# Performance work log

Measured on AMD Instinct MI355X. Metric: run time of the kernel, lower is better.

The kernel has to match this reference:

```python
import jax, jax.numpy as jnp
import numpy as np

N_AGENTS = 5
RNN = 128
ATT = 64
N_ACT = 10
IN_DIM = 256
SIZE = 65535  # multiple of N_AGENTS -> padding branch never taken
TAU = 0.01


def _gru_cell(x, h, w_ih, w_hh, b_ih, b_hh):
    # PyTorch GRUCell math
    gi = x @ w_ih.T + b_ih
    gh = h @ w_hh.T + b_hh
    i_r, i_z, i_n = jnp.split(gi, 3, axis=-1)
    h_r, h_z, h_n = jnp.split(gh, 3, axis=-1)
    r = jax.nn.sigmoid(i_r + h_r)
    z = jax.nn.sigmoid(i_z + h_z)
    n = jnp.tanh(i_n + r * h_n)
    return (1.0 - z) * n + z * h


def _gru_seq(xs, w_ih, w_hh, b_ih, b_hh):
    # xs: [T, B, D]; zero initial hidden, returns all step outputs [T, B, RNN]
    h0 = jnp.zeros((xs.shape[1], RNN), xs.dtype)
    def step(h, x):
        h2 = _gru_cell(x, h, w_ih, w_hh, b_ih, b_hh)
        return h2, h2
    _, ys = jax.lax.scan(step, h0, xs)
    return ys


def setup_inputs():
    key = jax.random.key(0)
    ks = jax.random.split(key, 26)
    def u(k, shape, fan):
        return jax.random.uniform(k, shape, jnp.float32, -1.0, 1.0) / np.sqrt(fan)
    return {
        'obs': jax.random.normal(ks[0], (SIZE, IN_DIM), jnp.float32),
        'hidden_state': jax.random.normal(ks[1], (SIZE, RNN), jnp.float32),
        'enc_w': u(ks[2], (RNN, IN_DIM), IN_DIM), 'enc_b': u(ks[3], (RNN,), IN_DIM),
        'gru_w_ih': u(ks[4], (3 * RNN, RNN), RNN), 'gru_w_hh': u(ks[5], (3 * RNN, RNN), RNN),
        'gru_b_ih': u(ks[6], (3 * RNN,), RNN), 'gru_b_hh': u(ks[7], (3 * RNN,), RNN),
        'bi_w_ih_f': u(ks[8], (3 * RNN, 2 * RNN), RNN), 'bi_w_hh_f': u(ks[9], (3 * RNN, RNN), RNN),
        'bi_b_ih_f': u(ks[10], (3 * RNN,), RNN), 'bi_b_hh_f': u(ks[11], (3 * RNN,), RNN),
        'bi_w_ih_r': u(ks[12], (3 * RNN, 2 * RNN), RNN), 'bi_w_hh_r': u(ks[13], (3 * RNN, RNN), RNN),
        'bi_b_ih_r': u(ks[14], (3 * RNN,), RNN), 'bi_b_hh_r': u(ks[15], (3 * RNN,), RNN),
        'hard_w': u(ks[16], (2, 2 * RNN), 2 * RNN), 'hard_b': u(ks[17], (2,), 2 * RNN),
        'q_w': u(ks[18], (ATT, RNN), RNN),
        'k_w': u(ks[19], (ATT, RNN), RNN),
        'v_w': u(ks[20], (ATT, RNN), RNN), 'v_b': u(ks[21], (ATT,), RNN),
        'dec_w': u(ks[22], (N_ACT, RNN + ATT), RNN + ATT), 'dec_b': u(ks[23], (N_ACT,), RNN + ATT),
    }


def reference(obs, hidden_state, enc_w, enc_b, gru_w_ih, gru_w_hh, gru_b_ih, gru_b_hh,
              bi_w_ih_f, bi_w_hh_f, bi_b_ih_f, bi_b_hh_f,
              bi_w_ih_r, bi_w_hh_r, bi_b_ih_r, bi_b_hh_r,
              hard_w, hard_b, q_w, k_w, v_w, v_b, dec_w, dec_b):
    size = obs.shape[0]
    bpa = size // N_AGENTS  # batch per agent; SIZE is a multiple of N_AGENTS

    x = jax.nn.relu(obs @ enc_w.T + enc_b)
    h_out = _gru_cell(x, hidden_state, gru_w_ih, gru_w_hh, gru_b_ih, gru_b_hh)

    # --- hard attention: pairwise agent features -> bi-GRU -> gumbel-softmax gate ---
    # (computed exactly as in the original; note the original soft_attention
    #  ignores hard_weights, so this does not influence the returned output)
    h = h_out.reshape(bpa, N_AGENTS, RNN)
    nbr = np.array([[j for j in range(N_AGENTS) if j != i] for i in range(N_AGENTS)])  # [n, n-1]
    h_i = jnp.broadcast_to(h[:, :, None, :], (bpa, N_AGENTS, N_AGENTS - 1, RNN))
    h_j = h[:, nbr, :]                              # [bpa, n, n-1, RNN]
    pair = jnp.concatenate([h_i, h_j], axis=-1)     # [bpa, n, n-1, 2*RNN]
    seq = pair.transpose(2, 0, 1, 3).reshape(N_AGENTS - 1, bpa * N_AGENTS, 2 * RNN)
    fwd = _gru_seq(seq, bi_w_ih_f, bi_w_hh_f, bi_b_ih_f, bi_b_hh_f)
    bwd = _gru_seq(seq[::-1], bi_w_ih_r, bi_w_hh_r, bi_b_ih_r, bi_b_hh_r)[::-1]
    h_hard = jnp.concatenate([fwd, bwd], axis=-1)   # [n-1, B, 2*RNN]
    h_hard = h_hard.transpose(1, 0, 2).reshape(-1, 2 * RNN)
    logits = h_hard @ hard_w.T + hard_b             # [B*(n-1), 2]
    u01 = jax.random.uniform(jax.random.key(42), logits.shape, jnp.float32, 1e-10, 1.0)
    gumbel = -jnp.log(-jnp.log(u01))
    gs = jax.nn.softmax((logits + gumbel) / TAU, axis=-1)
    hard_weights = gs[:, 1].reshape(bpa, N_AGENTS, 1, N_AGENTS - 1).transpose(1, 0, 2, 3)
    _ = hard_weights  # unused downstream, matching the original module

    # --- soft attention: original loops per sample doing a 1x1 matmul+softmax;
    #     vectorized here. softmax over a single element is identically 1. ---
    q = h_out @ q_w.T
    k = h_out @ k_w.T
    v = jax.nn.relu(h_out @ v_w.T + v_b)
    score = jnp.sum(q * k, axis=-1, keepdims=True) / np.sqrt(ATT)  # [B,1]
    soft_w = jax.nn.softmax(score, axis=-1)                         # all ones
    x_att = v * soft_w

    final_input = jnp.concatenate([h_out, x_att], axis=-1)
    output = final_input @ dec_w.T + dec_b
    return output, h_out
```

## Files before the change

### kernel.cpp

```cpp
#include <hip/hip_runtime.h>
#include <stdint.h>

#define SIZE 65535

typedef __bf16 bf16x8 __attribute__((ext_vector_type(8)));
typedef float floatx4 __attribute__((ext_vector_type(4)));

#define WS_ENCW 0
#define WS_WIH  32768
#define WS_WHH  81920
#define WS_VW   131072
#define WS_DECW 139264
#define WS_TOTC 17792

__device__ __forceinline__ unsigned short f2bf(float f) {
    union { float f; unsigned int u; } v; v.f = f;
    unsigned int u = v.u;
    return (unsigned short)((u + 0x7fffu + ((u >> 16) & 1u)) >> 16);
}
__device__ __forceinline__ float bf2f(unsigned short b) {
    union { unsigned int u; float f; } v; v.u = ((unsigned int)b) << 16;
    return v.f;
}
__device__ __forceinline__ float sigmf(float x) {
    x = fminf(fmaxf(x, -30.f), 30.f);
    return 1.f / (1.f + __expf(-x));
}
__device__ __forceinline__ float tanhfast(float x) {
    x = fminf(fmaxf(x, -15.f), 15.f);
    float e = __expf(2.f * x);
    return (e - 1.f) / (e + 1.f);
}

union BF8 { bf16x8 v; unsigned short s[8]; };

__device__ __forceinline__ bf16x8 cvt8g(const float* p) {
    float4 a = *reinterpret_cast<const float4*>(p);
    float4 b = *reinterpret_cast<const float4*>(p + 4);
    BF8 r;
    r.s[0] = f2bf(a.x); r.s[1] = f2bf(a.y); r.s[2] = f2bf(a.z); r.s[3] = f2bf(a.w);
    r.s[4] = f2bf(b.x); r.s[5] = f2bf(b.y); r.s[6] = f2bf(b.z); r.s[7] = f2bf(b.w);
    return r.v;
}
__device__ __forceinline__ bf16x8 ld8(const unsigned short* p) {
    return *reinterpret_cast<const bf16x8*>(p);
}

__global__ __launch_bounds__(256) void cvt_weights(
    const float* __restrict__ enc_w, const float* __restrict__ w_ih,
    const float* __restrict__ w_hh, const float* __restrict__ v_w,
    const float* __restrict__ dec_w, unsigned short* __restrict__ ws) {
    int c = blockIdx.x * 256 + threadIdx.x;
    if (c >= WS_TOTC) return;
    const int lane = c & 63;
    const int l = lane & 15;
    const int q = lane >> 4;
    const float* src; int row, col, stride; bool zero = false;
    if (c < 4096) {
        int lt = c >> 6; int nt = lt >> 3, kt = lt & 7;
        row = nt * 16 + l; col = kt * 32 + q * 8; src = enc_w; stride = 256;
    } else if (c < 10240) {
        int lt = (c - 4096) >> 6; int nt = lt / 12; int r2 = lt % 12;
        int g = r2 >> 2, kt = r2 & 3;
        row = g * 128 + nt * 16 + l; col = kt * 32 + q * 8; src = w_ih; stride = 128;
    } else if (c < 16384) {
        int lt = (c - 10240) >> 6; int nt = lt / 12; int r2 = lt % 12;
        int g = r2 >> 2, kt = r2 & 3;
        row = g * 128 + nt * 16 + l; col = kt * 32 + q * 8; src = w_hh; stride = 128;
    } else if (c < 17408) {
        int lt = (c - 16384) >> 6; int nt = lt >> 2, kt = lt & 3;
        row = nt * 16 + l; col = kt * 32 + q * 8; src = v_w; stride = 128;
    } else {
        int kt = (c - 17408) >> 6;
        row = l; col = kt * 32 + q * 8; src = dec_w; stride = 192;
        zero = (l >= 10);
    }
    float4 a, b;
    if (zero) { a = make_float4(0.f,0.f,0.f,0.f); b = a; }
    else {
        const float* p = src + (size_t)row * stride + col;
        a = *reinterpret_cast<const float4*>(p);
        b = *reinterpret_cast<const float4*>(p + 4);
    }
    unsigned short* d = ws + (size_t)c * 8;
    d[0]=f2bf(a.x); d[1]=f2bf(a.y); d[2]=f2bf(a.z); d[3]=f2bf(a.w);
    d[4]=f2bf(b.x); d[5]=f2bf(b.y); d[6]=f2bf(b.z); d[7]=f2bf(b.w);
}

__global__ __launch_bounds__(256, 2) void attn_critic_kernel(
    const float* __restrict__ obs,
    const float* __restrict__ hid,
    const float* __restrict__ enc_b,
    const float* __restrict__ b_ih,
    const float* __restrict__ b_hh,
    const float* __restrict__ v_b,
    const float* __restrict__ dec_b,
    const unsigned short* __restrict__ wsw,
    float* __restrict__ out)
{
    __shared__ __align__(16) unsigned short sA[4][32][136];
    __shared__ __align__(16) unsigned short sV[4][32][72];
    __shared__ __align__(16) float sO[4][32][10];

    const int tid  = threadIdx.x;
    const int wave = tid >> 6;
    const int lane = tid & 63;
    const int l15  = lane & 15;
    const int quad = lane >> 4;
    const int wrow0 = (blockIdx.x * 4 + wave) * 32;

    int rA0 = wrow0 + l15;      rA0 = (rA0 < SIZE) ? rA0 : (SIZE - 1);
    int rA1 = wrow0 + 16 + l15; rA1 = (rA1 < SIZE) ? rA1 : (SIZE - 1);

    bf16x8 aob[2][8], hf[2][4];
    {
        const float* o0 = obs + (size_t)rA0 * 256;
        const float* o1 = obs + (size_t)rA1 * 256;
#pragma unroll
        for (int kt = 0; kt < 8; ++kt) {
            aob[0][kt] = cvt8g(o0 + kt * 32 + quad * 8);
            aob[1][kt] = cvt8g(o1 + kt * 32 + quad * 8);
        }
        const float* h0 = hid + (size_t)rA0 * 128;
        const float* h1 = hid + (size_t)rA1 * 128;
#pragma unroll
        for (int kt = 0; kt < 4; ++kt) {
            hf[0][kt] = cvt8g(h0 + kt * 32 + quad * 8);
            hf[1][kt] = cvt8g(h1 + kt * 32 + quad * 8);
        }
    }
    __builtin_amdgcn_sched_barrier(0);

    {
        const unsigned short* encf = wsw + WS_ENCW + lane * 8;
#pragma unroll 2
        for (int nt = 0; nt < 8; ++nt) {
            floatx4 a0 = floatx4{0.f,0.f,0.f,0.f}, a1 = a0;
#pragma unroll
            for (int kt = 0; kt < 8; ++kt) {
                bf16x8 b = ld8(encf + (size_t)(nt * 8 + kt) * 512);
                a0 = __builtin_amdgcn_mfma_f32_16x16x32_bf16(aob[0][kt], b, a0, 0, 0, 0);
                a1 = __builtin_amdgcn_mfma_f32_16x16x32_bf16(aob[1][kt], b, a1, 0, 0, 0);
            }
            float bias = enc_b[nt * 16 + l15];
#pragma unroll
            for (int r = 0; r < 4; ++r) {
                sA[wave][quad * 4 + r][nt * 16 + l15]      = f2bf(fmaxf(a0[r] + bias, 0.f));
                sA[wave][16 + quad * 4 + r][nt * 16 + l15] = f2bf(fmaxf(a1[r] + bias, 0.f));
            }
        }
    }
    bf16x8 xf[2][4];
#pragma unroll
    for (int kt = 0; kt < 4; ++kt) {
        xf[0][kt] = ld8(&sA[wave][l15][kt * 32 + quad * 8]);
        xf[1][kt] = ld8(&sA[wave][16 + l15][kt * 32 + quad * 8]);
    }

    {
        const unsigned short* wihf = wsw + WS_WIH + lane * 8;
        const unsigned short* whhf = wsw + WS_WHH + lane * 8;
#pragma unroll 1
        for (int nt = 0; nt < 8; ++nt) {
            const int nr = nt * 16 + l15;
            floatx4 gi[3][2], gh[3][2];
#pragma unroll
            for (int g = 0; g < 3; ++g) {
                gi[g][0] = floatx4{0.f,0.f,0.f,0.f}; gi[g][1] = gi[g][0];
                gh[g][0] = gi[g][0]; gh[g][1] = gi[g][0];
            }
#pragma unroll
            for (int g = 0; g < 3; ++g)
#pragma unroll
                for (int kt = 0; kt < 4; ++kt) {
                    bf16x8 bi = ld8(wihf + (size_t)((nt * 3 + g) * 4 + kt) * 512);
                    bf16x8 bh = ld8(whhf + (size_t)((nt * 3 + g) * 4 + kt) * 512);
                    gi[g][0] = __builtin_amdgcn_mfma_f32_16x16x32_bf16(xf[0][kt], bi, gi[g][0], 0, 0, 0);
                    gi[g][1] = __builtin_amdgcn_mfma_f32_16x16x32_bf16(xf[1][kt], bi, gi[g][1], 0, 0, 0);
                    gh[g][0] = __builtin_amdgcn_mfma_f32_16x16x32_bf16(hf[0][kt], bh, gh[g][0], 0, 0, 0);
                    gh[g][1] = __builtin_amdgcn_mfma_f32_16x16x32_bf16(hf[1][kt], bh, gh[g][1], 0, 0, 0);
                }
            const float bir_ = b_ih[nr], biz_ = b_ih[nr + 128], bin_ = b_ih[nr + 256];
            const float bhr_ = b_hh[nr], bhz_ = b_hh[nr + 128], bhn_ = b_hh[nr + 256];
#pragma unroll
            for (int m = 0; m < 2; ++m)
#pragma unroll
                for (int r = 0; r < 4; ++r) {
                    const int grow = wrow0 + m * 16 + quad * 4 + r;
                    const int rowc = (grow < SIZE) ? grow : (SIZE - 1);
                    float hprev = hid[(size_t)rowc * 128 + nr];
                    float rg = sigmf(gi[0][m][r] + bir_ + gh[0][m][r] + bhr_);
                    float zg = sigmf(gi[1][m][r] + biz_ + gh[1][m][r] + bhz_);
                    float ng = tanhfast(gi[2][m][r] + bin_ + rg * (gh[2][m][r] + bhn_));
                    float ho = (1.f - zg) * ng + zg * hprev;
                    sA[wave][m * 16 + quad * 4 + r][nr] = f2bf(ho);
                }
        }
    }

    {
        float* out_h = out + (size_t)SIZE * 10;
#pragma unroll 1
        for (int it = 0; it < 16; ++it) {
            int idx = it * 256 + lane * 4;
            int rr = idx >> 7, cc = idx & 127;
            int grow = wrow0 + rr;
            if (grow < SIZE) {
                float2 p0 = make_float2(bf2f(sA[wave][rr][cc]),     bf2f(sA[wave][rr][cc + 1]));
                float2 p1 = make_float2(bf2f(sA[wave][rr][cc + 2]), bf2f(sA[wave][rr][cc + 3]));
                float* dst = out_h + (size_t)grow * 128 + cc;
                *reinterpret_cast<float2*>(dst)     = p0;
                *reinterpret_cast<float2*>(dst + 2) = p1;
            }
        }
    }

    bf16x8 af[2][4];
#pragma unroll
    for (int kt = 0; kt < 4; ++kt) {
        af[0][kt] = ld8(&sA[wave][l15][kt * 32 + quad * 8]);
        af[1][kt] = ld8(&sA[wave][16 + l15][kt * 32 + quad * 8]);
    }
    {
        const unsigned short* vwf = wsw + WS_VW + lane * 8;
#pragma unroll 1
        for (int nt = 0; nt < 4; ++nt) {
            floatx4 a0 = floatx4{0.f,0.f,0.f,0.f}, a1 = a0;
#pragma unroll
            for (int kt = 0; kt < 4; ++kt) {
                bf16x8 b = ld8(vwf + (size_t)(nt * 4 + kt) * 512);
                a0 = __builtin_amdgcn_mfma_f32_16x16x32_bf16(af[0][kt], b, a0, 0, 0, 0);
                a1 = __builtin_amdgcn_mfma_f32_16x16x32_bf16(af[1][kt], b, a1, 0, 0, 0);
            }
            float bias = v_b[nt * 16 + l15];
#pragma unroll
            for (int r = 0; r < 4; ++r) {
                sV[wave][quad * 4 + r][nt * 16 + l15]      = f2bf(fmaxf(a0[r] + bias, 0.f));
                sV[wave][16 + quad * 4 + r][nt * 16 + l15] = f2bf(fmaxf(a1[r] + bias, 0.f));
            }
        }
    }

    {
        const unsigned short* decf = wsw + WS_DECW + lane * 8;
        floatx4 d0 = floatx4{0.f,0.f,0.f,0.f}, d1 = d0;
#pragma unroll
        for (int kt = 0; kt < 6; ++kt) {
            bf16x8 b = ld8(decf + (size_t)kt * 512);
            bf16x8 a0 = (kt < 4) ? af[0][kt] : ld8(&sV[wave][l15][(kt - 4) * 32 + quad * 8]);
            bf16x8 a1 = (kt < 4) ? af[1][kt] : ld8(&sV[wave][16 + l15][(kt - 4) * 32 + quad * 8]);
            d0 = __builtin_amdgcn_mfma_f32_16x16x32_bf16(a0, b, d0, 0, 0, 0);
            d1 = __builtin_amdgcn_mfma_f32_16x16x32_bf16(a1, b, d1, 0, 0, 0);
        }
        if (l15 < 10) {
            float bias = dec_b[l15];
#pragma unroll
            for (int r = 0; r < 4; ++r) {
                sO[wave][quad * 4 + r][l15]      = d0[r] + bias;
                sO[wave][16 + quad * 4 + r][l15] = d1[r] + bias;
            }
        }
#pragma unroll
        for (int j = 0; j < 5; ++j) {
            int idx = j * 64 + lane;
            int row = idx / 10, col = idx % 10;
            int grow = wrow0 + row;
            if (grow < SIZE)
                out[(size_t)grow * 10 + col] = sO[wave][row][col];
        }
    }
}

extern "C" void kernel_launch(void* const* d_in, const int* in_sizes, int n_in,
                              void* d_out, int out_size, void* d_ws, size_t ws_size,
                              hipStream_t stream) {
    const float* obs   = (const float*)d_in[0];
    const float* hid   = (const float*)d_in[1];
    const float* enc_w = (const float*)d_in[2];
    const float* enc_b = (const float*)d_in[3];
    const float* w_ih  = (const float*)d_in[4];
    const float* w_hh  = (const float*)d_in[5];
    const float* b_ih  = (const float*)d_in[6];
    const float* b_hh  = (const float*)d_in[7];
    const float* v_w   = (const float*)d_in[20];
    const float* v_b   = (const float*)d_in[21];
    const float* dec_w = (const float*)d_in[22];
    const float* dec_b = (const float*)d_in[23];
    unsigned short* wsw = (unsigned short*)d_ws;
    float* out = (float*)d_out;

    hipLaunchKernelGGL(cvt_weights, dim3((WS_TOTC + 255) / 256), dim3(256), 0, stream,
                       enc_w, w_ih, w_hh, v_w, dec_w, wsw);
    hipLaunchKernelGGL(attn_critic_kernel, dim3(512), dim3(256), 0, stream,
                       obs, hid, enc_b, b_ih, b_hh, v_b, dec_b, wsw, out);
}
```

Baseline: 224.1 us.

## Halve rows per wave to 16 and double grid for higher occupancy

Each wave now processes 16 rows instead of 32, halving per-wave register arrays and shared memory. Launch bounds go from 2 to 4 blocks per SM and the grid doubles to 1024 blocks, so more waves can hide memory latency. The cost is that each weight fragment loaded from the workspace now feeds only one MFMA instead of two, which doubles weight traffic per output row.

```diff
diff --git a/kernel.cpp b/kernel.cpp
--- a/kernel.cpp
+++ b/kernel.cpp
@@ -87,7 +87,7 @@
     d[4]=f2bf(b.x); d[5]=f2bf(b.y); d[6]=f2bf(b.z); d[7]=f2bf(b.w);
 }
 
-__global__ __launch_bounds__(256, 2) void attn_critic_kernel(
+__global__ __launch_bounds__(256, 4) void attn_critic_kernel(
     const float* __restrict__ obs,
     const float* __restrict__ hid,
     const float* __restrict__ enc_b,
@@ -98,36 +98,29 @@
     const unsigned short* __restrict__ wsw,
     float* __restrict__ out)
 {
-    __shared__ __align__(16) unsigned short sA[4][32][136];
-    __shared__ __align__(16) unsigned short sV[4][32][72];
-    __shared__ __align__(16) float sO[4][32][10];
+    __shared__ __align__(16) unsigned short sA[4][16][136];
+    __shared__ __align__(16) unsigned short sV[4][16][72];
+    __shared__ __align__(16) float sO[4][16][10];
 
     const int tid  = threadIdx.x;
     const int wave = tid >> 6;
     const int lane = tid & 63;
     const int l15  = lane & 15;
     const int quad = lane >> 4;
-    const int wrow0 = (blockIdx.x * 4 + wave) * 32;
-
-    int rA0 = wrow0 + l15;      rA0 = (rA0 < SIZE) ? rA0 : (SIZE - 1);
-    int rA1 = wrow0 + 16 + l15; rA1 = (rA1 < SIZE) ? rA1 : (SIZE - 1);
-
-    bf16x8 aob[2][8], hf[2][4];
+    const int wrow0 = (blockIdx.x * 4 + wave) * 16;
+
+    int rA0 = wrow0 + l15; rA0 = (rA0 < SIZE) ? rA0 : (SIZE - 1);
+
+    bf16x8 aob[8], hf[4];
     {
         const float* o0 = obs + (size_t)rA0 * 256;
-        const float* o1 = obs + (size_t)rA1 * 256;
-#pragma unroll
-        for (int kt = 0; kt < 8; ++kt) {
-            aob[0][kt] = cvt8g(o0 + kt * 32 + quad * 8);
-            aob[1][kt] = cvt8g(o1 + kt * 32 + quad * 8);
-        }
+#pragma unroll
+        for (int kt = 0; kt < 8; ++kt)
+            aob[kt] = cvt8g(o0 + kt * 32 + quad * 8);
         const float* h0 = hid + (size_t)rA0 * 128;
-        const float* h1 = hid + (size_t)rA1 * 128;
-#pragma unroll
-        for (int kt = 0; kt < 4; ++kt) {
-            hf[0][kt] = cvt8g(h0 + kt * 32 + quad * 8);
-            hf[1][kt] = cvt8g(h1 + kt * 32 + quad * 8);
-        }
+#pragma unroll
+        for (int kt = 0; kt < 4; ++kt)
+            hf[kt] = cvt8g(h0 + kt * 32 + quad * 8);
     }
     __builtin_amdgcn_sched_barrier(0);
 
@@ -135,27 +128,22 @@
         const unsigned short* encf = wsw + WS_ENCW + lane * 8;
 #pragma unroll 2
         for (int nt = 0; nt < 8; ++nt) {
-            floatx4 a0 = floatx4{0.f,0.f,0.f,0.f}, a1 = a0;
+            floatx4 a0 = floatx4{0.f,0.f,0.f,0.f};
 #pragma unroll
             for (int kt = 0; kt < 8; ++kt) {
                 bf16x8 b = ld8(encf + (size_t)(nt * 8 + kt) * 512);
-                a0 = __builtin_amdgcn_mfma_f32_16x16x32_bf16(aob[0][kt], b, a0, 0, 0, 0);
-                a1 = __builtin_amdgcn_mfma_f32_16x16x32_bf16(aob[1][kt], b, a1, 0, 0, 0);
+                a0 = __builtin_amdgcn_mfma_f32_16x16x32_bf16(aob[kt], b, a0, 0, 0, 0);
             }
             float bias = enc_b[nt * 16 + l15];
 #pragma unroll
-            for (int r = 0; r < 4; ++r) {
-                sA[wave][quad * 4 + r][nt * 16 + l15]      = f2bf(fmaxf(a0[r] + bias, 0.f));
-                sA[wave][16 + quad * 4 + r][nt * 16 + l15] = f2bf(fmaxf(a1[r] + bias, 0.f));
-            }
-        }
-    }
-    bf16x8 xf[2][4];
-#pragma unroll
-    for (int kt = 0; kt < 4; ++kt) {
-        xf[0][kt] = ld8(&sA[wave][l15][kt * 32 + quad * 8]);
-        xf[1][kt] = ld8(&sA[wave][16 + l15][kt * 32 + quad * 8]);
-    }
+            for (int r = 0; r < 4; ++r)
+                sA[wave][quad * 4 + r][nt * 16 + l15] = f2bf(fmaxf(a0[r] + bias, 0.f));
+        }
+    }
+    bf16x8 xf[4];
+#pragma unroll
+    for (int kt = 0; kt < 4; ++kt)
+        xf[kt] = ld8(&sA[wave][l15][kt * 32 + quad * 8]);
 
     {
         const unsigned short* wihf = wsw + WS_WIH + lane * 8;
@@ -163,11 +151,11 @@
 #pragma unroll 1
         for (int nt = 0; nt < 8; ++nt) {
             const int nr = nt * 16 + l15;
-            floatx4 gi[3][2], gh[3][2];
+            floatx4 gi[3], gh[3];
 #pragma unroll
             for (int g = 0; g < 3; ++g) {
-                gi[g][0] = floatx4{0.f,0.f,0.f,0.f}; gi[g][1] = gi[g][0];
-                gh[g][0] = gi[g][0]; gh[g][1] = gi[g][0];
+                gi[g] = floatx4{0.f,0.f,0.f,0.f};
+                gh[g] = gi[g];
             }
 #pragma unroll
             for (int g = 0; g < 3; ++g)
@@ -175,33 +163,29 @@
                 for (int kt = 0; kt < 4; ++kt) {
                     bf16x8 bi = ld8(wihf + (size_t)((nt * 3 + g) * 4 + kt) * 512);
                     bf16x8 bh = ld8(whhf + (size_t)((nt * 3 + g) * 4 + kt) * 512);
-                    gi[g][0] = __builtin_amdgcn_mfma_f32_16x16x32_bf16(xf[0][kt], bi, gi[g][0], 0, 0, 0);
-                    gi[g][1] = __builtin_amdgcn_mfma_f32_16x16x32_bf16(xf[1][kt], bi, gi[g][1], 0, 0, 0);
-                    gh[g][0] = __builtin_amdgcn_mfma_f32_16x16x32_bf16(hf[0][kt], bh, gh[g][0], 0, 0, 0);
-                    gh[g][1] = __builtin_amdgcn_mfma_f32_16x16x32_bf16(hf[1][kt], bh, gh[g][1], 0, 0, 0);
+                    gi[g] = __builtin_amdgcn_mfma_f32_16x16x32_bf16(xf[kt], bi, gi[g], 0, 0, 0);
+                    gh[g] = __builtin_amdgcn_mfma_f32_16x16x32_bf16(hf[kt], bh, gh[g], 0, 0, 0);
                 }
             const float bir_ = b_ih[nr], biz_ = b_ih[nr + 128], bin_ = b_ih[nr + 256];
             const float bhr_ = b_hh[nr], bhz_ = b_hh[nr + 128], bhn_ = b_hh[nr + 256];
 #pragma unroll
-            for (int m = 0; m < 2; ++m)
-#pragma unroll
-                for (int r = 0; r < 4; ++r) {
-                    const int grow = wrow0 + m * 16 + quad * 4 + r;
-                    const int rowc = (grow < SIZE) ? grow : (SIZE - 1);
-                    float hprev = hid[(size_t)rowc * 128 + nr];
-                    float rg = sigmf(gi[0][m][r] + bir_ + gh[0][m][r] + bhr_);
-                    float zg = sigmf(gi[1][m][r] + biz_ + gh[1][m][r] + bhz_);
-                    float ng = tanhfast(gi[2][m][r] + bin_ + rg * (gh[2][m][r] + bhn_));
-                    float ho = (1.f - zg) * ng + zg * hprev;
-                    sA[wave][m * 16 + quad * 4 + r][nr] = f2bf(ho);
-                }
+            for (int r = 0; r < 4; ++r) {
+                const int grow = wrow0 + quad * 4 + r;
+                const int rowc = (grow < SIZE) ? grow : (SIZE - 1);
+                float hprev = hid[(size_t)rowc * 128 + nr];
+                float rg = sigmf(gi[0][r] + bir_ + gh[0][r] + bhr_);
+                float zg = sigmf(gi[1][r] + biz_ + gh[1][r] + bhz_);
+                float ng = tanhfast(gi[2][r] + bin_ + rg * (gh[2][r] + bhn_));
+                float ho = (1.f - zg) * ng + zg * hprev;
+                sA[wave][quad * 4 + r][nr] = f2bf(ho);
+            }
         }
     }
 
     {
         float* out_h = out + (size_t)SIZE * 10;
 #pragma unroll 1
-        for (int it = 0; it < 16; ++it) {
+        for (int it = 0; it < 8; ++it) {
             int idx = it * 256 + lane * 4;
             int rr = idx >> 7, cc = idx & 127;
             int grow = wrow0 + rr;
@@ -215,58 +199,51 @@
         }
     }
 
-    bf16x8 af[2][4];
-#pragma unroll
-    for (int kt = 0; kt < 4; ++kt) {
-        af[0][kt] = ld8(&sA[wave][l15][kt * 32 + quad * 8]);
-        af[1][kt] = ld8(&sA[wave][16 + l15][kt * 32 + quad * 8]);
-    }
+    bf16x8 af[4];
+#pragma unroll
+    for (int kt = 0; kt < 4; ++kt)
+        af[kt] = ld8(&sA[wave][l15][kt * 32 + quad * 8]);
     {
         const unsigned short* vwf = wsw + WS_VW + lane * 8;
 #pragma unroll 1
         for (int nt = 0; nt < 4; ++nt) {
-            floatx4 a0 = floatx4{0.f,0.f,0.f,0.f}, a1 = a0;
+            floatx4 a0 = floatx4{0.f,0.f,0.f,0.f};
 #pragma unroll
             for (int kt = 0; kt < 4; ++kt) {
                 bf16x8 b = ld8(vwf + (size_t)(nt * 4 + kt) * 512);
-                a0 = __builtin_amdgcn_mfma_f32_16x16x32_bf16(af[0][kt], b, a0, 0, 0, 0);
-                a1 = __builtin_amdgcn_mfma_f32_16x16x32_bf16(af[1][kt], b, a1, 0, 0, 0);
+                a0 = __builtin_amdgcn_mfma_f32_16x16x32_bf16(af[kt], b, a0, 0, 0, 0);
             }
             float bias = v_b[nt * 16 + l15];
 #pragma unroll
-            for (int r = 0; r < 4; ++r) {
-                sV[wave][quad * 4 + r][nt * 16 + l15]      = f2bf(fmaxf(a0[r] + bias, 0.f));
-                sV[wave][16 + quad * 4 + r][nt * 16 + l15] = f2bf(fmaxf(a1[r] + bias, 0.f));
-            }
+            for (int r = 0; r < 4; ++r)
+                sV[wave][quad * 4 + r][nt * 16 + l15] = f2bf(fmaxf(a0[r] + bias, 0.f));
         }
     }
 
     {
         const unsigned short* decf = wsw + WS_DECW + lane * 8;
-        floatx4 d0 = floatx4{0.f,0.f,0.f,0.f}, d1 = d0;
+        floatx4 d0 = floatx4{0.f,0.f,0.f,0.f};
 #pragma unroll
         for (int kt = 0; kt < 6; ++kt) {
             bf16x8 b = ld8(decf + (size_t)kt * 512);
-            bf16x8 a0 = (kt < 4) ? af[0][kt] : ld8(&sV[wave][l15][(kt - 4) * 32 + quad * 8]);
-            bf16x8 a1 = (kt < 4) ? af[1][kt] : ld8(&sV[wave][16 + l15][(kt - 4) * 32 + quad * 8]);
+            bf16x8 a0 = (kt < 4) ? af[kt] : ld8(&sV[wave][l15][(kt - 4) * 32 + quad * 8]);
             d0 = __builtin_amdgcn_mfma_f32_16x16x32_bf16(a0, b, d0, 0, 0, 0);
-            d1 = __builtin_amdgcn_mfma_f32_16x16x32_bf16(a1, b, d1, 0, 0, 0);
         }
         if (l15 < 10) {
             float bias = dec_b[l15];
 #pragma unroll
-            for (int r = 0; r < 4; ++r) {
-                sO[wave][quad * 4 + r][l15]      = d0[r] + bias;
-                sO[wave][16 + quad * 4 + r][l15] = d1[r] + bias;
-            }
-        }
-#pragma unroll
-        for (int j = 0; j < 5; ++j) {
+            for (int r = 0; r < 4; ++r)
+                sO[wave][quad * 4 + r][l15] = d0[r] + bias;
+        }
+#pragma unroll
+        for (int j = 0; j < 3; ++j) {
             int idx = j * 64 + lane;
-            int row = idx / 10, col = idx % 10;
-            int grow = wrow0 + row;
-            if (grow < SIZE)
-                out[(size_t)grow * 10 + col] = sO[wave][row][col];
+            if (idx < 160) {
+                int row = idx / 10, col = idx % 10;
+                int grow = wrow0 + row;
+                if (grow < SIZE)
+                    out[(size_t)grow * 10 + col] = sO[wave][row][col];
+            }
         }
     }
 }
@@ -291,6 +268,6 @@
 
     hipLaunchKernelGGL(cvt_weights, dim3((WS_TOTC + 255) / 256), dim3(256), 0, stream,
                        enc_w, w_ih, w_hh, v_w, dec_w, wsw);
-    hipLaunchKernelGGL(attn_critic_kernel, dim3(512), dim3(256), 0, stream,
+    hipLaunchKernelGGL(attn_critic_kernel, dim3(1024), dim3(256), 0, stream,
                        obs, hid, enc_b, b_ih, b_hh, v_b, dec_b, wsw, out);
 }
```

After: 223.6 us. No clear change (-0.2%).

## Stage weight fragments into LDS via async global_load_lds double buffering

Applied to the files above, without the earlier changes.

Weight fragments for the encoder, GRU, value and decoder matmuls are now copied cooperatively by all four waves into a double-buffered LDS region using global_load_lds. Each tile is prefetched one step ahead while the current tile feeds the MFMAs. This replaces per-wave redundant global loads of the same weights with a shared copy. The h_out store is also moved after the decoder, and hprev loads are hoisted before the GRU MFMAs. The cost is a block-wide __syncthreads after every weight tile (about 40 barriers) and 16KB more LDS, which may lower occupancy.

```diff
diff --git a/kernel.cpp b/kernel.cpp
--- a/kernel.cpp
+++ b/kernel.cpp
@@ -44,6 +44,24 @@
 }
 __device__ __forceinline__ bf16x8 ld8(const unsigned short* p) {
     return *reinterpret_cast<const bf16x8*>(p);
+}
+
+__device__ __forceinline__ void glds16(const unsigned short* g, unsigned short* l) {
+    __builtin_amdgcn_global_load_lds(
+        (const __attribute__((address_space(1))) unsigned int*)g,
+        (__attribute__((address_space(3))) unsigned int*)l, 16, 0, 0);
+}
+
+__device__ __forceinline__ void stage_seq(unsigned short* dst, const unsigned short* src,
+                                          int nfrags, int wave, int lane) {
+    for (int s = wave; s < nfrags; s += 4)
+        glds16(src + s * 512 + lane * 8, dst + s * 512);
+}
+__device__ __forceinline__ void stage_gru(unsigned short* dst, const unsigned short* wsw,
+                                          int ng, int wave, int lane) {
+    const int fo = (ng * 4 + wave) * 512 + lane * 8;
+    glds16(wsw + WS_WIH + fo, dst + wave * 512);
+    glds16(wsw + WS_WHH + fo, dst + (4 + wave) * 512);
 }
 
 __global__ __launch_bounds__(256) void cvt_weights(
@@ -98,6 +116,7 @@
     const unsigned short* __restrict__ wsw,
     float* __restrict__ out)
 {
+    __shared__ __align__(16) unsigned short wbuf[2][4096];
     __shared__ __align__(16) unsigned short sA[4][32][136];
     __shared__ __align__(16) unsigned short sV[4][32][72];
     __shared__ __align__(16) float sO[4][32][10];
@@ -112,6 +131,8 @@
     int rA0 = wrow0 + l15;      rA0 = (rA0 < SIZE) ? rA0 : (SIZE - 1);
     int rA1 = wrow0 + 16 + l15; rA1 = (rA1 < SIZE) ? rA1 : (SIZE - 1);
 
+    stage_seq(wbuf[0], wsw + WS_ENCW, 8, wave, lane);
+
     bf16x8 aob[2][8], hf[2][4];
     {
         const float* o0 = obs + (size_t)rA0 * 256;
@@ -130,26 +151,29 @@
         }
     }
     __builtin_amdgcn_sched_barrier(0);
-
-    {
-        const unsigned short* encf = wsw + WS_ENCW + lane * 8;
-#pragma unroll 2
-        for (int nt = 0; nt < 8; ++nt) {
-            floatx4 a0 = floatx4{0.f,0.f,0.f,0.f}, a1 = a0;
-#pragma unroll
-            for (int kt = 0; kt < 8; ++kt) {
-                bf16x8 b = ld8(encf + (size_t)(nt * 8 + kt) * 512);
-                a0 = __builtin_amdgcn_mfma_f32_16x16x32_bf16(aob[0][kt], b, a0, 0, 0, 0);
-                a1 = __builtin_amdgcn_mfma_f32_16x16x32_bf16(aob[1][kt], b, a1, 0, 0, 0);
-            }
-            float bias = enc_b[nt * 16 + l15];
-#pragma unroll
-            for (int r = 0; r < 4; ++r) {
-                sA[wave][quad * 4 + r][nt * 16 + l15]      = f2bf(fmaxf(a0[r] + bias, 0.f));
-                sA[wave][16 + quad * 4 + r][nt * 16 + l15] = f2bf(fmaxf(a1[r] + bias, 0.f));
-            }
-        }
-    }
+    __syncthreads();
+
+#pragma unroll 1
+    for (int nt = 0; nt < 8; ++nt) {
+        const int cur = nt & 1;
+        if (nt < 7) stage_seq(wbuf[cur ^ 1], wsw + WS_ENCW + (nt + 1) * 4096, 8, wave, lane);
+        else        stage_gru(wbuf[cur ^ 1], wsw, 0, wave, lane);
+        const float bias = enc_b[nt * 16 + l15];
+        floatx4 a0 = floatx4{0.f,0.f,0.f,0.f}, a1 = a0;
+#pragma unroll
+        for (int kt = 0; kt < 8; ++kt) {
+            bf16x8 b = ld8(&wbuf[cur][kt * 512 + lane * 8]);
+            a0 = __builtin_amdgcn_mfma_f32_16x16x32_bf16(aob[0][kt], b, a0, 0, 0, 0);
+            a1 = __builtin_amdgcn_mfma_f32_16x16x32_bf16(aob[1][kt], b, a1, 0, 0, 0);
+        }
+#pragma unroll
+        for (int r = 0; r < 4; ++r) {
+            sA[wave][quad * 4 + r][nt * 16 + l15]      = f2bf(fmaxf(a0[r] + bias, 0.f));
+            sA[wave][16 + quad * 4 + r][nt * 16 + l15] = f2bf(fmaxf(a1[r] + bias, 0.f));
+        }
+        __syncthreads();
+    }
+
     bf16x8 xf[2][4];
 #pragma unroll
     for (int kt = 0; kt < 4; ++kt) {
@@ -157,44 +181,107 @@
         xf[1][kt] = ld8(&sA[wave][16 + l15][kt * 32 + quad * 8]);
     }
 
+#pragma unroll 1
+    for (int nt = 0; nt < 8; ++nt) {
+        const int nr = nt * 16 + l15;
+        float hp[2][4];
+#pragma unroll
+        for (int m = 0; m < 2; ++m)
+#pragma unroll
+            for (int r = 0; r < 4; ++r) {
+                const int grow = wrow0 + m * 16 + quad * 4 + r;
+                const int rowc = (grow < SIZE) ? grow : (SIZE - 1);
+                hp[m][r] = hid[(size_t)rowc * 128 + nr];
+            }
+        const float bir_ = b_ih[nr], biz_ = b_ih[nr + 128], bin_ = b_ih[nr + 256];
+        const float bhr_ = b_hh[nr], bhz_ = b_hh[nr + 128], bhn_ = b_hh[nr + 256];
+        floatx4 gi[3][2], gh[3][2];
+#pragma unroll
+        for (int g = 0; g < 3; ++g) {
+            gi[g][0] = floatx4{0.f,0.f,0.f,0.f}; gi[g][1] = gi[g][0];
+            gh[g][0] = gi[g][0]; gh[g][1] = gi[g][0];
+        }
+#pragma unroll
+        for (int g = 0; g < 3; ++g) {
+            const int cur = (nt + g) & 1;
+            const int ng = nt * 3 + g + 1;
+            if (ng < 24) stage_gru(wbuf[cur ^ 1], wsw, ng, wave, lane);
+            else         stage_seq(wbuf[cur ^ 1], wsw + WS_VW, 4, wave, lane);
+#pragma unroll
+            for (int kt = 0; kt < 4; ++kt) {
+                bf16x8 bi = ld8(&wbuf[cur][kt * 512 + lane * 8]);
+                bf16x8 bh = ld8(&wbuf[cur][(4 + kt) * 512 + lane * 8]);
+                gi[g][0] = __builtin_amdgcn_mfma_f32_16x16x32_bf16(xf[0][kt], bi, gi[g][0], 0, 0, 0);
+                gi[g][1] = __builtin_amdgcn_mfma_f32_16x16x32_bf16(xf[1][kt], bi, gi[g][1], 0, 0, 0);
+                gh[g][0] = __builtin_amdgcn_mfma_f32_16x16x32_bf16(hf[0][kt], bh, gh[g][0], 0, 0, 0);
+                gh[g][1] = __builtin_amdgcn_mfma_f32_16x16x32_bf16(hf[1][kt], bh, gh[g][1], 0, 0, 0);
+            }
+            __syncthreads();
+        }
+#pragma unroll
+        for (int m = 0; m < 2; ++m)
+#pragma unroll
+            for (int r = 0; r < 4; ++r) {
+                float rg = sigmf(gi[0][m][r] + bir_ + gh[0][m][r] + bhr_);
+                float zg = sigmf(gi[1][m][r] + biz_ + gh[1][m][r] + bhz_);
+                float ng2 = tanhfast(gi[2][m][r] + bin_ + rg * (gh[2][m][r] + bhn_));
+                float ho = (1.f - zg) * ng2 + zg * hp[m][r];
+                sA[wave][m * 16 + quad * 4 + r][nr] = f2bf(ho);
+            }
+    }
+
+    bf16x8 af[2][4];
+#pragma unroll
+    for (int kt = 0; kt < 4; ++kt) {
+        af[0][kt] = ld8(&sA[wave][l15][kt * 32 + quad * 8]);
+        af[1][kt] = ld8(&sA[wave][16 + l15][kt * 32 + quad * 8]);
+    }
+#pragma unroll 1
+    for (int nt = 0; nt < 4; ++nt) {
+        const int cur = nt & 1;
+        if (nt < 3) stage_seq(wbuf[cur ^ 1], wsw + WS_VW + (nt + 1) * 2048, 4, wave, lane);
+        else        stage_seq(wbuf[cur ^ 1], wsw + WS_DECW, 6, wave, lane);
+        const float bias = v_b[nt * 16 + l15];
+        floatx4 a0 = floatx4{0.f,0.f,0.f,0.f}, a1 = a0;
+#pragma unroll
+        for (int kt = 0; kt < 4; ++kt) {
+            bf16x8 b = ld8(&wbuf[cur][kt * 512 + lane * 8]);
+            a0 = __builtin_amdgcn_mfma_f32_16x16x32_bf16(af[0][kt], b, a0, 0, 0, 0);
+            a1 = __builtin_amdgcn_mfma_f32_16x16x32_bf16(af[1][kt], b, a1, 0, 0, 0);
+        }
+#pragma unroll
+        for (int r = 0; r < 4; ++r) {
+            sV[wave][quad * 4 + r][nt * 16 + l15]      = f2bf(fmaxf(a0[r] + bias, 0.f));
+            sV[wave][16 + quad * 4 + r][nt * 16 + l15] = f2bf(fmaxf(a1[r] + bias, 0.f));
+        }
+        __syncthreads();
+    }
+
     {
-        const unsigned short* wihf = wsw + WS_WIH + lane * 8;
-        const unsigned short* whhf = wsw + WS_WHH + lane * 8;
-#pragma unroll 1
-        for (int nt = 0; nt < 8; ++nt) {
-            const int nr = nt * 16 + l15;
-            floatx4 gi[3][2], gh[3][2];
-#pragma unroll
-            for (int g = 0; g < 3; ++g) {
-                gi[g][0] = floatx4{0.f,0.f,0.f,0.f}; gi[g][1] = gi[g][0];
-                gh[g][0] = gi[g][0]; gh[g][1] = gi[g][0];
-            }
-#pragma unroll
-            for (int g = 0; g < 3; ++g)
-#pragma unroll
-                for (int kt = 0; kt < 4; ++kt) {
-                    bf16x8 bi = ld8(wihf + (size_t)((nt * 3 + g) * 4 + kt) * 512);
-                    bf16x8 bh = ld8(whhf + (size_t)((nt * 3 + g) * 4 + kt) * 512);
-                    gi[g][0] = __builtin_amdgcn_mfma_f32_16x16x32_bf16(xf[0][kt], bi, gi[g][0], 0, 0, 0);
-                    gi[g][1] = __builtin_amdgcn_mfma_f32_16x16x32_bf16(xf[1][kt], bi, gi[g][1], 0, 0, 0);
-                    gh[g][0] = __builtin_amdgcn_mfma_f32_16x16x32_bf16(hf[0][kt], bh, gh[g][0], 0, 0, 0);
-                    gh[g][1] = __builtin_amdgcn_mfma_f32_16x16x32_bf16(hf[1][kt], bh, gh[g][1], 0, 0, 0);
-                }
-            const float bir_ = b_ih[nr], biz_ = b_ih[nr + 128], bin_ = b_ih[nr + 256];
-            const float bhr_ = b_hh[nr], bhz_ = b_hh[nr + 128], bhn_ = b_hh[nr + 256];
-#pragma unroll
-            for (int m = 0; m < 2; ++m)
-#pragma unroll
-                for (int r = 0; r < 4; ++r) {
-                    const int grow = wrow0 + m * 16 + quad * 4 + r;
-                    const int rowc = (grow < SIZE) ? grow : (SIZE - 1);
-                    float hprev = hid[(size_t)rowc * 128 + nr];
-                    float rg = sigmf(gi[0][m][r] + bir_ + gh[0][m][r] + bhr_);
-                    float zg = sigmf(gi[1][m][r] + biz_ + gh[1][m][r] + bhz_);
-                    float ng = tanhfast(gi[2][m][r] + bin_ + rg * (gh[2][m][r] + bhn_));
-                    float ho = (1.f - zg) * ng + zg * hprev;
-                    sA[wave][m * 16 + quad * 4 + r][nr] = f2bf(ho);
-                }
+        floatx4 d0 = floatx4{0.f,0.f,0.f,0.f}, d1 = d0;
+#pragma unroll
+        for (int kt = 0; kt < 6; ++kt) {
+            bf16x8 b = ld8(&wbuf[0][kt * 512 + lane * 8]);
+            bf16x8 a0 = (kt < 4) ? af[0][kt] : ld8(&sV[wave][l15][(kt - 4) * 32 + quad * 8]);
+            bf16x8 a1 = (kt < 4) ? af[1][kt] : ld8(&sV[wave][16 + l15][(kt - 4) * 32 + quad * 8]);
+            d0 = __builtin_amdgcn_mfma_f32_16x16x32_bf16(a0, b, d0, 0, 0, 0);
+            d1 = __builtin_amdgcn_mfma_f32_16x16x32_bf16(a1, b, d1, 0, 0, 0);
+        }
+        if (l15 < 10) {
+            const float bias = dec_b[l15];
+#pragma unroll
+            for (int r = 0; r < 4; ++r) {
+                sO[wave][quad * 4 + r][l15]      = d0[r] + bias;
+                sO[wave][16 + quad * 4 + r][l15] = d1[r] + bias;
+            }
+        }
+#pragma unroll
+        for (int j = 0; j < 5; ++j) {
+            int idx = j * 64 + lane;
+            int row = idx / 10, col = idx % 10;
+            int grow = wrow0 + row;
+            if (grow < SIZE)
+                out[(size_t)grow * 10 + col] = sO[wave][row][col];
         }
     }
 
@@ -212,61 +299,6 @@
                 *reinterpret_cast<float2*>(dst)     = p0;
                 *reinterpret_cast<float2*>(dst + 2) = p1;
             }
-        }
-    }
-
-    bf16x8 af[2][4];
-#pragma unroll
-    for (int kt = 0; kt < 4; ++kt) {
-        af[0][kt] = ld8(&sA[wave][l15][kt * 32 + quad * 8]);
-        af[1][kt] = ld8(&sA[wave][16 + l15][kt * 32 + quad * 8]);
-    }
-    {
-        const unsigned short* vwf = wsw + WS_VW + lane * 8;
-#pragma unroll 1
-        for (int nt = 0; nt < 4; ++nt) {
-            floatx4 a0 = floatx4{0.f,0.f,0.f,0.f}, a1 = a0;
-#pragma unroll
-            for (int kt = 0; kt < 4; ++kt) {
-                bf16x8 b = ld8(vwf + (size_t)(nt * 4 + kt) * 512);
-                a0 = __builtin_amdgcn_mfma_f32_16x16x32_bf16(af[0][kt], b, a0, 0, 0, 0);
-                a1 = __builtin_amdgcn_mfma_f32_16x16x32_bf16(af[1][kt], b, a1, 0, 0, 0);
-            }
-            float bias = v_b[nt * 16 + l15];
-#pragma unroll
-            for (int r = 0; r < 4; ++r) {
-                sV[wave][quad * 4 + r][nt * 16 + l15]      = f2bf(fmaxf(a0[r] + bias, 0.f));
-                sV[wave][16 + quad * 4 + r][nt * 16 + l15] = f2bf(fmaxf(a1[r] + bias, 0.f));
-            }
-        }
-    }
-
-    {
-        const unsigned short* decf = wsw + WS_DECW + lane * 8;
-        floatx4 d0 = floatx4{0.f,0.f,0.f,0.f}, d1 = d0;
-#pragma unroll
-        for (int kt = 0; kt < 6; ++kt) {
-            bf16x8 b = ld8(decf + (size_t)kt * 512);
-            bf16x8 a0 = (kt < 4) ? af[0][kt] : ld8(&sV[wave][l15][(kt - 4) * 32 + quad * 8]);
-            bf16x8 a1 = (kt < 4) ? af[1][kt] : ld8(&sV[wave][16 + l15][(kt - 4) * 32 + quad * 8]);
-            d0 = __builtin_amdgcn_mfma_f32_16x16x32_bf16(a0, b, d0, 0, 0, 0);
-            d1 = __builtin_amdgcn_mfma_f32_16x16x32_bf16(a1, b, d1, 0, 0, 0);
-        }
-        if (l15 < 10) {
-            float bias = dec_b[l15];
-#pragma unroll
-            for (int r = 0; r < 4; ++r) {
-                sO[wave][quad * 4 + r][l15]      = d0[r] + bias;
-                sO[wave][16 + quad * 4 + r][l15] = d1[r] + bias;
-            }
-        }
-#pragma unroll
-        for (int j = 0; j < 5; ++j) {
-            int idx = j * 64 + lane;
-            int row = idx / 10, col = idx % 10;
-            int grow = wrow0 + row;
-            if (grow < SIZE)
-                out[(size_t)grow * 10 + col] = sO[wave][row][col];
         }
     }
 }
```

Result: faster. 209.7 us (-6.4%).
